# Performance work log

Hardware: AMD Instinct MI355X
Metric: run time of the kernel (lower is better)

The kernel has to match this reference:

```python
import jax, jax.numpy as jnp
import numpy as np

N_EMBD = 768
HEAD_SIZE = 64

def setup_inputs() -> dict:
    key = jax.random.key(0)
    ks = jax.random.split(key, 9)
    B, S = 8, 2048
    scale = 1.0 / np.sqrt(N_EMBD)
    return {
        "q": jax.random.normal(ks[0], (B, S, N_EMBD), jnp.float32),
        "k": jax.random.normal(ks[1], (B, S, N_EMBD), jnp.float32),
        "v": jax.random.normal(ks[2], (B, S, N_EMBD), jnp.float32),
        "Wq": jax.random.normal(ks[3], (N_EMBD, HEAD_SIZE), jnp.float32) * scale,
        "bq": jnp.zeros((HEAD_SIZE,), jnp.float32),
        "Wk": jax.random.normal(ks[4], (N_EMBD, HEAD_SIZE), jnp.float32) * scale,
        "bk": jnp.zeros((HEAD_SIZE,), jnp.float32),
        "Wv": jax.random.normal(ks[5], (N_EMBD, HEAD_SIZE), jnp.float32) * scale,
        "bv": jnp.zeros((HEAD_SIZE,), jnp.float32),
    }

def reference(q, k, v, Wq, bq, Wk, bk, Wv, bv):
    # NOTE: original scales by sqrt(C) where C = n_embd (input dim), not head_size.
    C = q.shape[-1]
    qi = q @ Wq + bq  # [B,S,H]
    ki = k @ Wk + bk
    vi = v @ Wv + bv
    att = jnp.einsum('bsh,bth->bst', qi, ki) / jnp.sqrt(jnp.float32(C))
    att = jax.nn.softmax(att, axis=-1)
    out = jnp.einsum('bst,bth->bsh', att, vi)
    return out
```

## Files before the change

kernel.cpp:

```cpp
#include <hip/hip_runtime.h>

#define Bn 8
#define Sn 2048
#define Cn 768
#define Hn 64
#define BS (Bn * Sn)

typedef __attribute__((ext_vector_type(8))) short bf16x8;
typedef __attribute__((ext_vector_type(4))) float f32x4;

__device__ __forceinline__ unsigned short f2bf(float x) {
  unsigned int u = __builtin_bit_cast(unsigned int, x);
  u += 0x7FFFu + ((u >> 16) & 1u);
  return (unsigned short)(u >> 16);
}

__global__ __launch_bounds__(256) void wconv(const float* __restrict__ Wq,
                                             const float* __restrict__ Wk,
                                             const float* __restrict__ Wv,
                                             unsigned short* __restrict__ Wt) {
  int idx = blockIdx.x * 256 + threadIdx.x;
  int mat = idx / (Cn * Hn);
  int rem = idx - mat * (Cn * Hn);
  int c = rem / Hn, h = rem - c * Hn;
  const float* W = (mat == 0) ? Wq : (mat == 1) ? Wk : Wv;
  Wt[mat * (Hn * Cn) + h * Cn + c] = f2bf(W[rem]);
}

__global__ __launch_bounds__(256) void proj(const float* __restrict__ q,
                                            const float* __restrict__ k,
                                            const float* __restrict__ v,
                                            const float* __restrict__ bq,
                                            const float* __restrict__ bk,
                                            const float* __restrict__ bv,
                                            const unsigned short* __restrict__ Wt,
                                            unsigned short* __restrict__ qi,
                                            unsigned short* __restrict__ ki,
                                            unsigned short* __restrict__ vi) {
  const int mat  = blockIdx.x >> 8;
  const int row0 = (blockIdx.x & 255) * 64;
  const float* X    = (mat == 0) ? q  : (mat == 1) ? k  : v;
  const float* bias = (mat == 0) ? bq : (mat == 1) ? bk : bv;
  unsigned short* Y = (mat == 0) ? qi : (mat == 1) ? ki : vi;
  const unsigned short* Wm = Wt + mat * (Hn * Cn);
  const float scale = (mat == 0) ? 0.03608439182435161f : 1.0f;

  __shared__ __align__(16) unsigned char Xs[64 * 1536];
  __shared__ __align__(16) unsigned char Ws[2][64 * 128];

  const int tid  = threadIdx.x;
  const int lane = tid & 63;
  const int w    = tid >> 6;
  const int col  = lane & 15;
  const int grp  = lane >> 4;

  const float* Xblk = X + (size_t)row0 * Cn;
#pragma unroll 8
  for (int i = 0; i < 48; ++i) {
    int f   = i * 256 + tid;
    int row = f / 192;
    int cf4 = f - row * 192;
    float4 xv = *(const float4*)(Xblk + (size_t)f * 4);
    ushort4 hv;
    hv.x = f2bf(xv.x); hv.y = f2bf(xv.y); hv.z = f2bf(xv.z); hv.w = f2bf(xv.w);
    *(ushort4*)(Xs + row * 1536 + ((cf4 * 8) ^ ((row & 7) << 4))) = hv;
  }
  const int wr_ = tid >> 2;
  const int wp_ = tid & 3;
  const unsigned short* Wrow = Wm + (size_t)wr_ * Cn + wp_ * 16;
  const int wo0 = wr_ * 128 + ((wp_ * 32) ^ ((wr_ & 7) << 4));
  const int wo1 = wr_ * 128 + (((wp_ * 32) + 16) ^ ((wr_ & 7) << 4));
  *(uint4*)(Ws[0] + wo0) = *(const uint4*)(Wrow);
  *(uint4*)(Ws[0] + wo1) = *(const uint4*)(Wrow + 8);
  __syncthreads();

  f32x4 acc[4] = {};
  const int rloc = w * 16 + col;
  const int xswz = (rloc & 7) << 4;

  for (int c = 0; c < 12; ++c) {
    uint4 wra, wrb;
    if (c < 11) {
      wra = *(const uint4*)(Wrow + (c + 1) * 64);
      wrb = *(const uint4*)(Wrow + (c + 1) * 64 + 8);
    }
    const unsigned char* Wb = Ws[c & 1];
#pragma unroll
    for (int ks = 0; ks < 2; ++ks) {
      bf16x8 a = *(const bf16x8*)(Xs + rloc * 1536 + ((c * 128 + ks * 64 + grp * 16) ^ xswz));
#pragma unroll
      for (int nf = 0; nf < 4; ++nf) {
        int wc = nf * 16 + col;
        bf16x8 bfr = *(const bf16x8*)(Wb + wc * 128 + ((ks * 64 + grp * 16) ^ ((wc & 7) << 4)));
        acc[nf] = __builtin_amdgcn_mfma_f32_16x16x32_bf16(a, bfr, acc[nf], 0, 0, 0);
      }
    }
    if (c < 11) {
      unsigned char* Wn = Ws[(c + 1) & 1];
      *(uint4*)(Wn + wo0) = wra;
      *(uint4*)(Wn + wo1) = wrb;
      __syncthreads();
    }
  }

#pragma unroll
  for (int nf = 0; nf < 4; ++nf) {
    int h = nf * 16 + col;
    float bb = bias[h];
#pragma unroll
    for (int r2 = 0; r2 < 4; ++r2) {
      int row = row0 + w * 16 + grp * 4 + r2;
      Y[(size_t)row * Hn + h] = f2bf((acc[nf][r2] + bb) * scale);
    }
  }
}

template <int SPLIT>
__global__ __launch_bounds__(256) void attn(const unsigned short* __restrict__ qi,
                                            const unsigned short* __restrict__ ki,
                                            const unsigned short* __restrict__ vi,
                                            float* __restrict__ pacc,
                                            float* __restrict__ pm,
                                            float* __restrict__ pl,
                                            float* __restrict__ out,
                                            int tpb) {
  const int bq    = blockIdx.x & 255;
  const int split = blockIdx.x >> 8;
  const int b  = bq >> 5;
  const int s0 = (bq & 31) * 64;
  const int t0 = split * tpb;
  const unsigned short* Qb = qi + ((size_t)b * Sn + s0) * Hn;
  const unsigned short* Kb = ki + (size_t)b * Sn * Hn;
  const unsigned short* Vb = vi + (size_t)b * Sn * Hn;

  __shared__ __align__(16) unsigned char Ks[64 * 128];
  __shared__ __align__(16) unsigned char Vt[64 * 128];
  __shared__ __align__(16) unsigned char Ps[4 * 16 * 128];

  const int tid  = threadIdx.x;
  const int lane = tid & 63;
  const int w    = tid >> 6;
  const int col  = lane & 15;
  const int grp  = lane >> 4;

  bf16x8 qa[2];
#pragma unroll
  for (int ks2 = 0; ks2 < 2; ++ks2)
    qa[ks2] = *(const bf16x8*)(Qb + (size_t)(w * 16 + col) * Hn + ks2 * 32 + grp * 8);

  f32x4 acc[4] = {};
  float m[4], l[4];
#pragma unroll
  for (int r = 0; r < 4; ++r) { m[r] = -1e30f; l[r] = 0.0f; }

  for (int t = t0; t < t0 + tpb; ++t) {
    const unsigned short* Kt = Kb + t * 64 * Hn;
    const unsigned short* Vg = Vb + t * 64 * Hn;
    __syncthreads();
    {
      int kr = tid >> 2, p = tid & 3;
      const uint4* src = (const uint4*)(Kt + kr * Hn);
      uint4 a  = src[p * 2];
      uint4 b2 = src[p * 2 + 1];
      *(uint4*)(Ks + kr * 128 + ((p * 32) ^ ((kr & 7) << 4)))        = a;
      *(uint4*)(Ks + kr * 128 + (((p * 32) + 16) ^ ((kr & 7) << 4))) = b2;
    }
    {
      int kp = tid >> 3;
      int dg = tid & 7;
      uint4 v0 = *(const uint4*)(Vg + (2 * kp) * Hn + dg * 8);
      uint4 v1 = *(const uint4*)(Vg + (2 * kp + 1) * Hn + dg * 8);
      const unsigned short* a0 = (const unsigned short*)&v0;
      const unsigned short* a1 = (const unsigned short*)&v1;
#pragma unroll
      for (int j0 = 0; j0 < 8; ++j0) {
        int j = (j0 + dg) & 7;
        int d = dg * 8 + j;
        unsigned int pk = (unsigned int)a0[j] | ((unsigned int)a1[j] << 16);
        *(unsigned int*)(Vt + d * 128 + ((4 * kp) ^ ((d & 7) << 4))) = pk;
      }
    }
    __syncthreads();
    f32x4 sf[4] = {};
#pragma unroll
    for (int ks2 = 0; ks2 < 2; ++ks2) {
#pragma unroll
      for (int nf = 0; nf < 4; ++nf) {
        int kr = nf * 16 + col;
        bf16x8 bfr = *(const bf16x8*)(Ks + kr * 128 + ((ks2 * 64 + grp * 16) ^ ((kr & 7) << 4)));
        sf[nf] = __builtin_amdgcn_mfma_f32_16x16x32_bf16(qa[ks2], bfr, sf[nf], 0, 0, 0);
      }
    }
    float mn[4], fs[4];
#pragma unroll
    for (int r = 0; r < 4; ++r) {
      float mx = fmaxf(fmaxf(sf[0][r], sf[1][r]), fmaxf(sf[2][r], sf[3][r]));
#pragma unroll
      for (int off = 1; off < 16; off <<= 1)
        mx = fmaxf(mx, __shfl_xor(mx, off, 64));
      mn[r] = fmaxf(m[r], mx);
      fs[r] = __expf(m[r] - mn[r]);
      m[r]  = mn[r];
    }
#pragma unroll
    for (int nf = 0; nf < 4; ++nf)
#pragma unroll
      for (int r = 0; r < 4; ++r)
        sf[nf][r] = __expf(sf[nf][r] - mn[r]);
#pragma unroll
    for (int r = 0; r < 4; ++r) {
      float sm = sf[0][r] + sf[1][r] + sf[2][r] + sf[3][r];
#pragma unroll
      for (int off = 1; off < 16; off <<= 1)
        sm += __shfl_xor(sm, off, 64);
      l[r] = l[r] * fs[r] + sm;
    }
#pragma unroll
    for (int nf = 0; nf < 4; ++nf) {
#pragma unroll
      for (int r = 0; r < 4; ++r) {
        acc[nf][r] *= fs[r];
        int prow = grp * 4 + r;
        int key  = nf * 16 + col;
        *(unsigned short*)(Ps + w * 2048 + prow * 128 + ((key * 2) ^ ((prow & 7) << 4))) =
            f2bf(sf[nf][r]);
      }
    }
#pragma unroll
    for (int kk = 0; kk < 2; ++kk) {
      bf16x8 pa = *(const bf16x8*)(Ps + w * 2048 + col * 128 +
                                   ((kk * 64 + grp * 16) ^ ((col & 7) << 4)));
#pragma unroll
      for (int nf = 0; nf < 4; ++nf) {
        int dr = nf * 16 + col;
        bf16x8 bv = *(const bf16x8*)(Vt + dr * 128 + ((kk * 64 + grp * 16) ^ ((dr & 7) << 4)));
        acc[nf] = __builtin_amdgcn_mfma_f32_16x16x32_bf16(pa, bv, acc[nf], 0, 0, 0);
      }
    }
  }
  if (SPLIT) {
    const size_t sb = (size_t)split * BS + (size_t)b * Sn;
#pragma unroll
    for (int nf = 0; nf < 4; ++nf) {
#pragma unroll
      for (int r = 0; r < 4; ++r) {
        int row = s0 + w * 16 + grp * 4 + r;
        pacc[(sb + row) * Hn + nf * 16 + col] = acc[nf][r];
      }
    }
    if (col == 0) {
#pragma unroll
      for (int r = 0; r < 4; ++r) {
        int row = s0 + w * 16 + grp * 4 + r;
        pm[sb + row] = m[r];
        pl[sb + row] = l[r];
      }
    }
  } else {
#pragma unroll
    for (int nf = 0; nf < 4; ++nf) {
#pragma unroll
      for (int r = 0; r < 4; ++r) {
        int row = s0 + w * 16 + grp * 4 + r;
        out[((size_t)b * Sn + row) * Hn + nf * 16 + col] = acc[nf][r] / l[r];
      }
    }
  }
}

__global__ __launch_bounds__(256) void combine(const float* __restrict__ pacc,
                                               const float* __restrict__ pm,
                                               const float* __restrict__ pl,
                                               float* __restrict__ out,
                                               int nsplit) {
  int gid = blockIdx.x * 256 + threadIdx.x;
  int gr  = gid >> 4;
  int dq  = (gid & 15) * 4;
  float M = -1e30f;
  for (int s = 0; s < nsplit; ++s) M = fmaxf(M, pm[(size_t)s * BS + gr]);
  float L = 0.0f;
  float4 o = make_float4(0.f, 0.f, 0.f, 0.f);
  for (int s = 0; s < nsplit; ++s) {
    float wgt = __expf(pm[(size_t)s * BS + gr] - M);
    L += pl[(size_t)s * BS + gr] * wgt;
    float4 p = *(const float4*)(pacc + ((size_t)s * BS + gr) * Hn + dq);
    o.x += p.x * wgt; o.y += p.y * wgt; o.z += p.z * wgt; o.w += p.w * wgt;
  }
  float inv = 1.0f / L;
  float4 r = make_float4(o.x * inv, o.y * inv, o.z * inv, o.w * inv);
  *(float4*)(out + (size_t)gr * Hn + dq) = r;
}

extern "C" void kernel_launch(void* const* d_in, const int* in_sizes, int n_in,
                              void* d_out, int out_size, void* d_ws, size_t ws_size,
                              hipStream_t stream) {
  const float* q  = (const float*)d_in[0];
  const float* k  = (const float*)d_in[1];
  const float* v  = (const float*)d_in[2];
  const float* Wq = (const float*)d_in[3];
  const float* bq = (const float*)d_in[4];
  const float* Wk = (const float*)d_in[5];
  const float* bk = (const float*)d_in[6];
  const float* Wv = (const float*)d_in[7];
  const float* bv = (const float*)d_in[8];
  float* out = (float*)d_out;

  unsigned short* Wt = (unsigned short*)d_ws;
  unsigned short* qi = Wt + 3 * Hn * Cn;
  unsigned short* ki = qi + (size_t)BS * Hn;
  unsigned short* vi = ki + (size_t)BS * Hn;
  float* pacc = (float*)(vi + (size_t)BS * Hn);

  const size_t base_bytes = (size_t)(3 * Hn * Cn + 3 * (size_t)BS * Hn) * 2;
  const size_t avail = (ws_size > base_bytes) ? ws_size - base_bytes : 0;

  int nsplit = 4;
  while (nsplit > 1 &&
         (size_t)nsplit * ((size_t)BS * Hn * 4 + 2 * (size_t)BS * 4) > avail)
    nsplit >>= 1;
  bool direct = ((size_t)nsplit * ((size_t)BS * Hn * 4 + 2 * (size_t)BS * 4) > avail);

  float* pm = pacc + (size_t)nsplit * BS * Hn;
  float* pl = pm + (size_t)nsplit * BS;

  wconv<<<dim3((3 * Cn * Hn) / 256), dim3(256), 0, stream>>>(Wq, Wk, Wv, Wt);
  proj<<<dim3(768), dim3(256), 0, stream>>>(q, k, v, bq, bk, bv, Wt, qi, ki, vi);
  if (direct) {
    attn<0><<<dim3(256), dim3(256), 0, stream>>>(qi, ki, vi, nullptr, nullptr, nullptr, out, 32);
  } else {
    attn<1><<<dim3(256 * nsplit), dim3(256), 0, stream>>>(qi, ki, vi, pacc, pm, pl, nullptr,
                                                          32 / nsplit);
    combine<<<dim3(BS * 16 / 256), dim3(256), 0, stream>>>(pacc, pm, pl, out, nsplit);
  }
}
```

Measured before the change: 101.7 us.

## Stream projection inputs via async global-to-LDS loads with double buffering

The projection kernel no longer stages the whole 64x768 input tile as bf16 in LDS before computing. It now streams 64-column fp32 chunks of X, plus the matching W chunks, with async global_load_lds into double-buffered, XOR-swizzled LDS, and converts to bf16 when it reads the MFMA operands. This cuts LDS use sharply, which should allow more resident blocks, and overlaps loading the next chunk with the current MFMAs. In exchange the fp32-to-bf16 conversion is repeated on each operand read, and correctness relies on the barrier waiting for the async LDS loads to finish.

```diff
diff --git a/kernel.cpp b/kernel.cpp
--- a/kernel.cpp
+++ b/kernel.cpp
@@ -13,6 +13,12 @@
   unsigned int u = __builtin_bit_cast(unsigned int, x);
   u += 0x7FFFu + ((u >> 16) & 1u);
   return (unsigned short)(u >> 16);
+}
+
+__device__ __forceinline__ void gload_lds16(const void* g, void* l) {
+  __builtin_amdgcn_global_load_lds(
+      (const __attribute__((address_space(1))) unsigned int*)g,
+      (__attribute__((address_space(3))) unsigned int*)l, 16, 0, 0);
 }
 
 __global__ __launch_bounds__(256) void wconv(const float* __restrict__ Wq,
@@ -45,8 +51,8 @@
   const unsigned short* Wm = Wt + mat * (Hn * Cn);
   const float scale = (mat == 0) ? 0.03608439182435161f : 1.0f;
 
-  __shared__ __align__(16) unsigned char Xs[64 * 1536];
-  __shared__ __align__(16) unsigned char Ws[2][64 * 128];
+  __shared__ __align__(16) float          Xf[2][4096];
+  __shared__ __align__(16) unsigned short Wl[2][4096];
 
   const int tid  = threadIdx.x;
   const int lane = tid & 63;
@@ -54,52 +60,60 @@
   const int col  = lane & 15;
   const int grp  = lane >> 4;
 
-  const float* Xblk = X + (size_t)row0 * Cn;
-#pragma unroll 8
-  for (int i = 0; i < 48; ++i) {
-    int f   = i * 256 + tid;
-    int row = f / 192;
-    int cf4 = f - row * 192;
-    float4 xv = *(const float4*)(Xblk + (size_t)f * 4);
-    ushort4 hv;
-    hv.x = f2bf(xv.x); hv.y = f2bf(xv.y); hv.z = f2bf(xv.z); hv.w = f2bf(xv.w);
-    *(ushort4*)(Xs + row * 1536 + ((cf4 * 8) ^ ((row & 7) << 4))) = hv;
-  }
-  const int wr_ = tid >> 2;
-  const int wp_ = tid & 3;
-  const unsigned short* Wrow = Wm + (size_t)wr_ * Cn + wp_ * 16;
-  const int wo0 = wr_ * 128 + ((wp_ * 32) ^ ((wr_ & 7) << 4));
-  const int wo1 = wr_ * 128 + (((wp_ * 32) + 16) ^ ((wr_ & 7) << 4));
-  *(uint4*)(Ws[0] + wo0) = *(const uint4*)(Wrow);
-  *(uint4*)(Ws[0] + wo1) = *(const uint4*)(Wrow + 8);
-  __syncthreads();
+  const float* xsrc[4];
+#pragma unroll
+  for (int j = 0; j < 4; ++j) {
+    int sidx = j * 256 + tid;
+    int row  = sidx >> 4;
+    int cf4  = (sidx & 15) ^ (row & 15);
+    xsrc[j]  = X + (size_t)(row0 + row) * Cn + cf4 * 4;
+  }
+  const unsigned short* wsrc[2];
+#pragma unroll
+  for (int j = 0; j < 2; ++j) {
+    int sidx = j * 256 + tid;
+    int h    = sidx >> 3;
+    int pd   = (sidx & 7) ^ (h & 7);
+    wsrc[j]  = Wm + (size_t)h * Cn + pd * 8;
+  }
+
+#pragma unroll
+  for (int j = 0; j < 4; ++j) gload_lds16(xsrc[j], &Xf[0][(j * 256 + w * 64) * 4]);
+#pragma unroll
+  for (int j = 0; j < 2; ++j) gload_lds16(wsrc[j], &Wl[0][(j * 256 + w * 64) * 8]);
 
   f32x4 acc[4] = {};
   const int rloc = w * 16 + col;
-  const int xswz = (rloc & 7) << 4;
 
   for (int c = 0; c < 12; ++c) {
-    uint4 wra, wrb;
+    const int buf = c & 1;
+    __syncthreads();
     if (c < 11) {
-      wra = *(const uint4*)(Wrow + (c + 1) * 64);
-      wrb = *(const uint4*)(Wrow + (c + 1) * 64 + 8);
-    }
-    const unsigned char* Wb = Ws[c & 1];
+      const int nb = buf ^ 1;
+#pragma unroll
+      for (int j = 0; j < 4; ++j)
+        gload_lds16(xsrc[j] + (c + 1) * 64, &Xf[nb][(j * 256 + w * 64) * 4]);
+#pragma unroll
+      for (int j = 0; j < 2; ++j)
+        gload_lds16(wsrc[j] + (c + 1) * 64, &Wl[nb][(j * 256 + w * 64) * 8]);
+    }
 #pragma unroll
     for (int ks = 0; ks < 2; ++ks) {
-      bf16x8 a = *(const bf16x8*)(Xs + rloc * 1536 + ((c * 128 + ks * 64 + grp * 16) ^ xswz));
+      const int cf0 = ks * 8 + grp * 2;
+      float4 a0 = *(const float4*)&Xf[buf][(rloc * 16 + (cf0 ^ col)) * 4];
+      float4 a1 = *(const float4*)&Xf[buf][(rloc * 16 + ((cf0 + 1) ^ col)) * 4];
+      bf16x8 av;
+      av[0] = (short)f2bf(a0.x); av[1] = (short)f2bf(a0.y);
+      av[2] = (short)f2bf(a0.z); av[3] = (short)f2bf(a0.w);
+      av[4] = (short)f2bf(a1.x); av[5] = (short)f2bf(a1.y);
+      av[6] = (short)f2bf(a1.z); av[7] = (short)f2bf(a1.w);
+      const int p = ks * 4 + grp;
 #pragma unroll
       for (int nf = 0; nf < 4; ++nf) {
-        int wc = nf * 16 + col;
-        bf16x8 bfr = *(const bf16x8*)(Wb + wc * 128 + ((ks * 64 + grp * 16) ^ ((wc & 7) << 4)));
-        acc[nf] = __builtin_amdgcn_mfma_f32_16x16x32_bf16(a, bfr, acc[nf], 0, 0, 0);
-      }
-    }
-    if (c < 11) {
-      unsigned char* Wn = Ws[(c + 1) & 1];
-      *(uint4*)(Wn + wo0) = wra;
-      *(uint4*)(Wn + wo1) = wrb;
-      __syncthreads();
+        int h = nf * 16 + col;
+        bf16x8 bfr = *(const bf16x8*)&Wl[buf][(h * 8 + (p ^ (h & 7))) * 8];
+        acc[nf] = __builtin_amdgcn_mfma_f32_16x16x32_bf16(av, bfr, acc[nf], 0, 0, 0);
+      }
     }
   }
 
```

Result: faster. 91.17 us (-10.3%).
